# Kernel optimization log

Measured on AMD Instinct MI355X. Metric: run time of the kernel, lower is better.

## Reference

```python
import jax, jax.numpy as jnp
import numpy as np

KEEP_ID, DEL_ID, PAD_ID, STOP_ID, ANNO_ID = 1, 2, 0, 102, 103
V, E, H = 21128, 768, 768
B, T = 8, 256
S = T + 1  # org/simp length; S = T+1 guarantees counters never go out of range


def setup_inputs() -> dict:
    key = jax.random.key(0)
    ks = jax.random.split(key, 16)
    def p(i, shape, scale):
        return jax.random.normal(ks[i], shape, jnp.float32) * scale
    return {
        "input_edits": jax.random.randint(ks[0], (B, T), 0, V),
        "org_ids": jax.random.randint(ks[1], (B, S), 0, V),
        "simp_sent": jax.random.randint(ks[2], (B, S), 0, V),
        "h0": jax.random.normal(ks[3], (B, H), jnp.float32),
        "c0": jax.random.normal(ks[4], (B, H), jnp.float32),
        "encoder_outputs_org": jax.random.normal(ks[5], (B, S, E), jnp.float32),
        "emb": p(6, (V, E), 0.02),
        "Wih_e": p(7, (4 * H, E), 0.03), "Whh_e": p(8, (4 * H, H), 0.03), "b_e": jnp.zeros((4 * H,), jnp.float32),
        "Wih_w": p(9, (4 * H, E), 0.03), "Whh_w": p(10, (4 * H, H), 0.03), "b_w": jnp.zeros((4 * H,), jnp.float32),
        "W_attn": p(11, (H, H), 0.03),
        "W_align": p(12, (H, E), 0.03),
        "W_mlp": p(13, (E, 4 * H), 0.03), "b_mlp": jnp.zeros((E,), jnp.float32),
        "W_out": p(14, (V, E), 0.02), "b_out": jnp.zeros((V,), jnp.float32),
    }


def lstm(x, h0, c0, Wih, Whh, b):
    # x: [B,T,E]; single-layer batch_first LSTM, torch gate order (i,f,g,o)
    def step(carry, xt):
        h, c = carry
        g = xt @ Wih.T + h @ Whh.T + b
        i, f, gg, o = jnp.split(g, 4, axis=-1)
        c2 = jax.nn.sigmoid(f) * c + jax.nn.sigmoid(i) * jnp.tanh(gg)
        h2 = jax.nn.sigmoid(o) * jnp.tanh(c2)
        return (h2, c2), h2
    (hT, cT), hs = jax.lax.scan(step, (h0, c0), jnp.swapaxes(x, 0, 1))
    return jnp.swapaxes(hs, 0, 1), hT, cT


def reference(input_edits, org_ids, simp_sent, h0, c0, encoder_outputs_org,
              emb, Wih_e, Whh_e, b_e, Wih_w, Whh_w, b_w,
              W_attn, W_align, W_mlp, b_mlp, W_out, b_out):
    bsz, nsteps = input_edits.shape
    enc = jnp.tanh(encoder_outputs_org @ W_align.T)            # [B,S,H]
    out_edits, hT, cT = lstm(emb[input_edits], h0, c0, Wih_e, Whh_e, b_e)  # [B,T,H]
    out_words, _, _ = lstm(emb[simp_sent], h0, c0, Wih_w, Whh_w, b_w)      # [B,S,H]

    key = out_edits @ W_attn.T                                  # [B,T,H]
    attn = jax.nn.softmax(jnp.einsum('bth,bsh->bts', key, enc), axis=-1)
    ctx = jnp.einsum('bts,bsh->bth', attn, enc)                 # [B,T,H]

    # counter recurrence (pre-update counters are used for the gathers at step t)
    gold = jnp.swapaxes(input_edits[:, 1:], 0, 1)               # [T-1, B]
    bidx = jnp.arange(bsz)

    def cstep(carry, a):
        kd, ki, an = carry
        kd2 = kd + ((a == KEEP_ID) | (a == DEL_ID)).astype(kd.dtype)
        not_special = (a != DEL_ID) & (a != STOP_ID) & (a != PAD_ID)
        ki2 = ki + not_special.astype(ki.dtype)
        is_ins = not_special & (a != KEEP_ID)
        next_is_anno = org_ids[bidx, an + 1] == ANNO_ID
        an2 = jnp.where(is_ins & next_is_anno, an + 1, jnp.maximum(kd2, an))
        return (kd2, ki2, an2), (ki, an)

    z = jnp.zeros((bsz,), jnp.int32)
    _, (ki_seq, an_seq) = jax.lax.scan(cstep, (z, z, z), gold)
    ki_bt = jnp.swapaxes(ki_seq, 0, 1)                          # [B,T-1]
    an_bt = jnp.swapaxes(an_seq, 0, 1)                          # [B,T-1]

    c = jnp.take_along_axis(enc, an_bt[:, :, None], axis=1)        # [B,T-1,H]
    c_word = jnp.take_along_axis(out_words, ki_bt[:, :, None], axis=1)  # [B,T-1,H]

    Tm1 = nsteps - 1
    feat = jnp.concatenate([out_edits[:, :Tm1], ctx[:, :Tm1], c, c_word], axis=-1)  # [B,T-1,4H]
    mlp = jnp.tanh(feat @ W_mlp.T + b_mlp)                      # [B,T-1,E]
    logp = jax.nn.log_softmax(mlp @ W_out.T + b_out, axis=-1)   # [B,T-1,V]
    return logp, hT, cT
```

## Files before the change

### kernel.cpp

```cpp
#include <hip/hip_runtime.h>
#include <hip/hip_bf16.h>

typedef short s16x8 __attribute__((ext_vector_type(8)));
typedef float f32x4 __attribute__((ext_vector_type(4)));
typedef unsigned short u16;
typedef unsigned short u16x4 __attribute__((ext_vector_type(4)));
typedef unsigned long long u64;
typedef unsigned long long u64x2 __attribute__((ext_vector_type(2)));

__device__ __forceinline__ u16 f2bf(float f) {
  __hip_bfloat16 h = __float2bfloat16(f);
  u16 u;
  __builtin_memcpy(&u, &h, sizeof(u));
  return u;
}
__device__ __forceinline__ float bf2f(u16 u) {
  unsigned int x = ((unsigned int)u) << 16;
  float f;
  __builtin_memcpy(&f, &x, 4);
  return f;
}

__device__ __forceinline__ unsigned int a_ld32(const unsigned int* p) {
  return __hip_atomic_load(p, __ATOMIC_RELAXED, __HIP_MEMORY_SCOPE_AGENT);
}
__device__ __forceinline__ u64 a_ld64(const u64* p) {
  return __hip_atomic_load(p, __ATOMIC_RELAXED, __HIP_MEMORY_SCOPE_AGENT);
}
__device__ __forceinline__ void a_st32(unsigned int* p, unsigned int v) {
  __hip_atomic_store(p, v, __ATOMIC_RELAXED, __HIP_MEMORY_SCOPE_AGENT);
}

__device__ __forceinline__ void gload16(const void* g, void* l) {
  __builtin_amdgcn_global_load_lds(
      (const __attribute__((address_space(1))) unsigned int*)g,
      (__attribute__((address_space(3))) unsigned int*)l, 16, 0, 0);
}

template<int CBF16, int GATHER, int TANHA, int BIAS, int SWAPXY>
__global__ __launch_bounds__(256) void gemm_bt(
    const u16* __restrict__ A, const u16* __restrict__ B,
    const float* __restrict__ bias, void* __restrict__ Cv,
    const int* __restrict__ ids,
    int M, int N, int K, int lda, int ldb, int ldc,
    long sAz, long sBz, long sCz, int rpb, long cbs,
    const int* __restrict__ ids2, const float* __restrict__ bias2, int dM)
{
  __shared__ u16 sA[4096];
  __shared__ u16 sB[4096];
  const int tid = threadIdx.x;
  const int z = blockIdx.z;
  if (z) {
    if (dM) M += dM;
    if (ids2) ids = ids2;
    if (bias2) bias = bias2;
  }
  const int m0 = (SWAPXY ? blockIdx.x : blockIdx.y) * 128;
  const int n0 = (SWAPXY ? blockIdx.y : blockIdx.x) * 128;
  const u16* Ab = A + z * sAz;
  const u16* Bb = B + z * sBz;
  const int w = tid >> 6, lane = tid & 63;
  const int wr = w >> 1, wc = w & 1;
  const int lr = lane & 15, lk = lane >> 4;
  f32x4 acc[4][4] = {};
  const int e0 = tid * 8, e1 = e0 + 2048;
  const int r0 = e0 >> 5, c0 = e0 & 31;
  const int r1 = e1 >> 5, c1 = e1 & 31;
  long arow0, arow1;
  if (GATHER) {
    int i0 = m0 + r0; if (i0 >= M) i0 = M - 1;
    int i1 = m0 + r1; if (i1 >= M) i1 = M - 1;
    arow0 = (long)ids[i0] * lda;
    arow1 = (long)ids[i1] * lda;
  } else {
    arow0 = (long)(m0 + r0) * lda;
    arow1 = (long)(m0 + r1) * lda;
  }
  const long brow0 = (long)(n0 + r0) * ldb;
  const long brow1 = (long)(n0 + r1) * ldb;
  char* sAc = (char*)sA;
  char* sBc = (char*)sB;
  const size_t cb = (size_t)w * 1024;
  for (int kt = 0; kt < K; kt += 32) {
    __syncthreads();
    gload16(Ab + arow0 + kt + c0, sAc + cb);
    gload16(Ab + arow1 + kt + c1, sAc + 4096 + cb);
    gload16(Bb + brow0 + kt + c0, sBc + cb);
    gload16(Bb + brow1 + kt + c1, sBc + 4096 + cb);
    __syncthreads();
    s16x8 af[4], bf[4];
#pragma unroll
    for (int i = 0; i < 4; i++) {
      af[i] = *(const s16x8*)&sA[(wr*64 + i*16 + lr)*32 + lk*8];
      bf[i] = *(const s16x8*)&sB[(wc*64 + i*16 + lr)*32 + lk*8];
    }
#pragma unroll
    for (int mi = 0; mi < 4; mi++)
#pragma unroll
      for (int ni = 0; ni < 4; ni++)
        acc[mi][ni] = __builtin_amdgcn_mfma_f32_16x16x32_bf16(af[mi], bf[ni], acc[mi][ni], 0, 0, 0);
  }
#pragma unroll
  for (int mi = 0; mi < 4; mi++) {
#pragma unroll
    for (int ni = 0; ni < 4; ni++) {
#pragma unroll
      for (int r = 0; r < 4; r++) {
        int gm = m0 + wr*64 + mi*16 + lk*4 + r;
        int gn = n0 + wc*64 + ni*16 + lr;
        if (gm < M && gn < N) {
          float v = acc[mi][ni][r];
          if (BIAS) v += bias[gn];
          if (TANHA) v = tanhf(v);
          long ci = z * sCz + (long)(gm / rpb) * cbs + (long)(gm % rpb) * ldc + gn;
          if (CBF16) ((u16*)Cv)[ci] = f2bf(v);
          else       ((float*)Cv)[ci] = v;
        }
      }
    }
  }
}

__global__ __launch_bounds__(256) void cast_pre(
    const float* __restrict__ emb,
    const float* __restrict__ Wihe, u16* __restrict__ Wihe_bf,
    const float* __restrict__ Wihw, u16* __restrict__ Wihw_bf,
    const float* __restrict__ Walign, u16* __restrict__ Walign_bf,
    const float* __restrict__ encoder, u16* __restrict__ encd_bf,
    u16* __restrict__ gath_bf,
    const int* __restrict__ input_edits, const int* __restrict__ simp_sent,
    const int* __restrict__ org_ids,
    int* __restrict__ ki_bt, int* __restrict__ an_bt,
    unsigned int* __restrict__ tags)
{
  int r = blockIdx.x;
  if (r == 13312) {
    int b = threadIdx.x;
    tags[b] = 0;
    if (b >= 8) return;
    int kd = 0, ki = 0, an = 0;
    for (int t = 0; t < 255; t++) {
      int a = input_edits[b * 256 + t + 1];
      ki_bt[b * 255 + t] = ki;
      an_bt[b * 255 + t] = an;
      int kd2 = kd + ((a == 1) || (a == 2) ? 1 : 0);
      int ns = (a != 2) && (a != 102) && (a != 0);
      int ki2 = ki + (ns ? 1 : 0);
      int is_ins = ns && (a != 1);
      int nia = (org_ids[b * 257 + an + 1] == 103);
      int mx = (kd2 > an) ? kd2 : an;
      int an2 = (is_ins && nia) ? (an + 1) : mx;
      kd = kd2; ki = ki2; an = an2;
    }
    return;
  }
  const float* src; u16* dst; int valid, cols;
  if (r < 3072)                   { src=Wihe + (long)r*768;   dst=Wihe_bf + (long)r*768;   valid=1; cols=768; }
  else if ((r -= 3072) < 3072)    { src=Wihw + (long)r*768;   dst=Wihw_bf + (long)r*768;   valid=1; cols=768; }
  else if ((r -= 3072) < 768)     { src=Walign + (long)r*768; dst=Walign_bf + (long)r*768; valid=1; cols=768; }
  else if ((r -= 768) < 2176)     { src=encoder + (long)r*768; dst=encd_bf + (long)r*768;  valid=(r<2056); cols=768; }
  else if ((r -= 2176) < 2048)    { src=emb + (long)input_edits[r]*768; dst=gath_bf + (long)r*768; valid=1; cols=768; }
  else { r -= 2048;                 int ok=(r<2056);
                                    src=emb + (ok ? (long)simp_sent[r]*768 : 0); 
                                    dst=gath_bf + (long)(2048+r)*768; valid=ok; cols=768; }
  for (int c = threadIdx.x; c < cols; c += 256) {
    float v = valid ? src[c] : 0.f;
    dst[c] = f2bf(v);
  }
}

__global__ __launch_bounds__(256, 1) void lstm_persist(
    const float* __restrict__ Whh_e, const float* __restrict__ Whh_w,
    const float* __restrict__ xW_e, const float* __restrict__ xW_w,
    const float* __restrict__ h0, const float* __restrict__ c0,
    u16* __restrict__ hglob, unsigned int* __restrict__ tags,
    u16* __restrict__ out_e, u16* __restrict__ out_w,
    float* __restrict__ out_tail,
    const float* __restrict__ Wout, u16* __restrict__ Wout_bf,
    const float* __restrict__ Wmlp, u16* __restrict__ Wmlp_bf,
    const float* __restrict__ Wattn, u16* __restrict__ Wattn_bf,
    const u16* __restrict__ enc_bf, u16* __restrict__ encT_bf)
{
  const int wg = blockIdx.x;
  const int tid = threadIdx.x;

  __shared__ u16 ldsh[12288];
  __shared__ float Gbuf[16][4][2][16];

  if (wg >= 48) {
    const int swg = wg - 48;
    u16 (*tile)[33] = (u16(*)[33])ldsh;
    const int TOT = 21248 + 768 + 768 + 1728;
    for (int u = swg; u < TOT; u += 208) {
      if (u < 21248) {
        const float* src = Wout + (long)u * 768;
        u16* dst = Wout_bf + (long)u * 768;
        bool ok = (u < 21128);
        for (int c = tid; c < 768; c += 256)
          dst[c] = f2bf(ok ? src[c] : 0.f);
      } else if (u < 22016) {
        int r = u - 21248;
        const float* src = Wmlp + (long)r * 3072;
        u16* dst = Wmlp_bf + (long)r * 3072;
        for (int c = tid; c < 3072; c += 256)
          dst[c] = f2bf(src[c]);
      } else if (u < 22784) {
        int r = u - 22016;
        const float* src = Wattn + (long)r * 768;
        u16* dst = Wattn_bf + (long)r * 768;
        for (int c = tid; c < 768; c += 256)
          dst[c] = f2bf(src[c]);
      } else {
        int tau = u - 22784;
        int s0 = (tau % 9) * 32;
        int rem = tau / 9;
        int hh0 = (rem % 24) * 32;
        int b = rem / 24;
        const int tx = tid & 31, ty = tid >> 5;
#pragma unroll
        for (int i = 0; i < 32; i += 8) {
          int s = s0 + ty + i;
          u16 v = (s < 257) ? enc_bf[((long)b * 384 + s) * 768 + hh0 + tx] : (u16)0;
          tile[ty + i][tx] = v;
        }
        __syncthreads();
#pragma unroll
        for (int i = 0; i < 32; i += 8) {
          int h = hh0 + ty + i;
          encT_bf[((long)b * 768 + h) * 288 + s0 + tx] = tile[tx][ty + i];
        }
        __syncthreads();
      }
    }
    return;
  }

  const int l = wg / 24, grp = wg % 24;
  const int u0 = grp * 32;
  const int w = tid >> 6, lane = tid & 63;
  const int c16 = lane & 15, half = lane >> 4;
  const int uh = w >> 1, g0 = (w & 1) * 2;

  s16x8 wfrag[2][24];
  {
    const float* Wbase = l ? Whh_w : Whh_e;
#pragma unroll
    for (int g = 0; g < 2; g++) {
      const float* Wsrc = Wbase + (long)((g0 + g) * 768 + u0 + uh * 16 + c16) * 768 + half * 8;
#pragma unroll
      for (int s = 0; s < 24; s++) {
        float4 f0 = *(const float4*)(Wsrc + s * 32);
        float4 f1 = *(const float4*)(Wsrc + s * 32 + 4);
        s16x8 v;
        v[0]=f2bf(f0.x); v[1]=f2bf(f0.y); v[2]=f2bf(f0.z); v[3]=f2bf(f0.w);
        v[4]=f2bf(f1.x); v[5]=f2bf(f1.y); v[6]=f2bf(f1.z); v[7]=f2bf(f1.w);
        wfrag[g][s] = v;
      }
    }
  }

  const int ub = tid >> 4, j2 = (tid & 15) * 2;
  const int uA = u0 + j2;
  float creg0 = 0.f, creg1 = 0.f;
  if (tid < 128) {
    creg0 = c0[ub * 768 + uA];
    creg1 = c0[ub * 768 + uA + 1];
  }

  u16* hg = hglob + l * 24576;
  unsigned int* tg = tags + l * 64;
  const int swA = uA ^ ((ub & 7) << 3);

  if (tid < 128) {
    float v0 = h0[ub * 768 + uA], v1 = h0[ub * 768 + uA + 1];
    u16 h0a = f2bf(v0), h0b = f2bf(v1);
    u16 l0a = f2bf(v0 - bf2f(h0a)), l0b = f2bf(v1 - bf2f(h0b));
    a_st32((unsigned int*)&hg[ub * 768 + swA],
           (unsigned int)h0a | ((unsigned int)h0b << 16));
    a_st32((unsigned int*)&hg[(ub + 8) * 768 + swA],
           (unsigned int)l0a | ((unsigned int)l0b << 16));
  }
  __syncthreads();
  if (tid == 0) a_st32(&tg[grp], 1u);

  const int trow = l ? 257 : 256;
  const float* xrb = (l ? xW_w : xW_e) + ((long)ub * trow) * 3072 + uA;
  u16* outp = (l ? out_w : out_e) + (long)ub * 256 * 768 + uA;
  float2 xq0, xq1, xq2, xq3;
  if (tid < 128) {
    xq0 = *(const float2*)&xrb[0];
    xq1 = *(const float2*)&xrb[768];
    xq2 = *(const float2*)&xrb[1536];
    xq3 = *(const float2*)&xrb[2304];
  }

  for (int t = 0; t < 256; t++) {
    float2 nx0, nx1, nx2, nx3;
    if (tid < 128) {
      const float* xn = xrb + (long)(t + 1) * 3072;
      nx0 = *(const float2*)&xn[0];
      nx1 = *(const float2*)&xn[768];
      nx2 = *(const float2*)&xn[1536];
      nx3 = *(const float2*)&xn[2304];
    }

    {
      const unsigned int tgt = (unsigned int)(t + 1);
      const unsigned int* tp = tg + (t & 1) * 32;
      const bool need = (lane < 24) && (lane != grp);
      while (true) {
        unsigned int v = need ? a_ld32(&tp[lane]) : tgt;
        if (!__any(v < tgt)) break;
        __builtin_amdgcn_s_sleep(1);
      }
      asm volatile("" ::: "memory");
    }

    {
      const u64* hs8 = (const u64*)(hg + (t & 1) * 12288);
#pragma unroll
      for (int i = 0; i < 6; i++) {
        const int idx = i * 256 + tid;
        u64 a = a_ld64(&hs8[idx * 2 + 0]);
        u64 b = a_ld64(&hs8[idx * 2 + 1]);
        u64x2 vv; vv[0] = a; vv[1] = b;
        *(u64x2*)&ldsh[idx * 8] = vv;
      }
    }
    __syncthreads();

    f32x4 acc0 = {}, acc1 = {};
#pragma unroll
    for (int s = 0; s < 24; s++) {
      const int off = (c16 * 768 + s * 32 + half * 8) ^ ((c16 & 7) << 3);
      s16x8 a = *(const s16x8*)&ldsh[off];
      acc0 = __builtin_amdgcn_mfma_f32_16x16x32_bf16(a, wfrag[0][s], acc0, 0, 0, 0);
      acc1 = __builtin_amdgcn_mfma_f32_16x16x32_bf16(a, wfrag[1][s], acc1, 0, 0, 0);
    }
#pragma unroll
    for (int r = 0; r < 4; r++) {
      Gbuf[half * 4 + r][g0 + 0][uh][c16] = acc0[r];
      Gbuf[half * 4 + r][g0 + 1][uh][c16] = acc1[r];
    }
    __syncthreads();

    unsigned int hip = 0;
    float h20 = 0.f, h21 = 0.f, c20 = 0.f, c21 = 0.f;
    if (tid < 128) {
      const int uh0 = j2 >> 4, uc0 = j2 & 15;
      const int uc1 = (j2 + 1) & 15;
      float gi0 = Gbuf[ub][0][uh0][uc0] + Gbuf[ub + 8][0][uh0][uc0] + xq0.x;
      float gf0 = Gbuf[ub][1][uh0][uc0] + Gbuf[ub + 8][1][uh0][uc0] + xq1.x;
      float gg0 = Gbuf[ub][2][uh0][uc0] + Gbuf[ub + 8][2][uh0][uc0] + xq2.x;
      float go0 = Gbuf[ub][3][uh0][uc0] + Gbuf[ub + 8][3][uh0][uc0] + xq3.x;
      float gi1 = Gbuf[ub][0][uh0][uc1] + Gbuf[ub + 8][0][uh0][uc1] + xq0.y;
      float gf1 = Gbuf[ub][1][uh0][uc1] + Gbuf[ub + 8][1][uh0][uc1] + xq1.y;
      float gg1 = Gbuf[ub][2][uh0][uc1] + Gbuf[ub + 8][2][uh0][uc1] + xq2.y;
      float go1 = Gbuf[ub][3][uh0][uc1] + Gbuf[ub + 8][3][uh0][uc1] + xq3.y;
      float si0 = 1.f / (1.f + expf(-gi0)), si1 = 1.f / (1.f + expf(-gi1));
      float sf0 = 1.f / (1.f + expf(-gf0)), sf1 = 1.f / (1.f + expf(-gf1));
      float so0 = 1.f / (1.f + expf(-go0)), so1 = 1.f / (1.f + expf(-go1));
      c20 = sf0 * creg0 + si0 * tanhf(gg0);
      c21 = sf1 * creg1 + si1 * tanhf(gg1);
      h20 = so0 * tanhf(c20);
      h21 = so1 * tanhf(c21);
      creg0 = c20; creg1 = c21;
      u16 hiA = f2bf(h20), hiB = f2bf(h21);
      u16 loA = f2bf(h20 - bf2f(hiA)), loB = f2bf(h21 - bf2f(hiB));
      hip = (unsigned int)hiA | ((unsigned int)hiB << 16);
      unsigned int lop = (unsigned int)loA | ((unsigned int)loB << 16);
      u16* hb = hg + ((t + 1) & 1) * 12288;
      a_st32((unsigned int*)&hb[ub * 768 + swA], hip);
      a_st32((unsigned int*)&hb[(ub + 8) * 768 + swA], lop);
      xq0 = nx0; xq1 = nx1; xq2 = nx2; xq3 = nx3;
    }
    __syncthreads();
    if (tid == 0)
      a_st32(&tg[((t + 1) & 1) * 32 + grp], (unsigned int)(t + 2));

    if (tid < 128) {
      *(unsigned int*)&outp[(long)t * 768] = hip;
      if (l == 0 && t == 255) {
        *(float2*)&out_tail[43101120 + ub * 768 + uA] = make_float2(h20, h21);
        *(float2*)&out_tail[43107264 + ub * 768 + uA] = make_float2(c20, c21);
      }
    }
  }
}

__global__ __launch_bounds__(256) void softmax_k(
    const float* __restrict__ scores, u16* __restrict__ attn)
{
  const int row = blockIdx.x;
  const float* src = scores + (long)row * 288;
  u16* dst = attn + (long)row * 288;
  const int tid = threadIdx.x;
  float v0 = (tid < 257) ? src[tid] : -1e30f;
  float v1 = (tid + 256 < 257) ? src[tid + 256] : -1e30f;
  float mx = fmaxf(v0, v1);
  for (int o = 32; o; o >>= 1) mx = fmaxf(mx, __shfl_xor(mx, o));
  __shared__ float sm[4];
  __shared__ float ss[4];
  if ((tid & 63) == 0) sm[tid >> 6] = mx;
  __syncthreads();
  mx = fmaxf(fmaxf(sm[0], sm[1]), fmaxf(sm[2], sm[3]));
  float e0 = (tid < 257) ? expf(v0 - mx) : 0.f;
  float e1 = (tid + 256 < 257) ? expf(v1 - mx) : 0.f;
  float s = e0 + e1;
  for (int o = 32; o; o >>= 1) s += __shfl_xor(s, o);
  if ((tid & 63) == 0) ss[tid >> 6] = s;
  __syncthreads();
  s = ss[0] + ss[1] + ss[2] + ss[3];
  float inv = 1.f / s;
  dst[tid] = f2bf(e0 * inv);
  if (tid + 256 < 288) dst[tid + 256] = f2bf(e1 * inv);
}

__global__ __launch_bounds__(256) void feat_k(
    const u16* __restrict__ oute, const u16* __restrict__ ctx,
    const u16* __restrict__ encb, const u16* __restrict__ outw,
    const int* __restrict__ ki_bt, const int* __restrict__ an_bt,
    u16* __restrict__ feat)
{
  int q = blockIdx.x * 256 + threadIdx.x;
  int m = q / 768, qq = q - m * 768;
  int seg = qq / 192, off = (qq - seg * 192) * 4;
  u16x4 v = {0, 0, 0, 0};
  if (m < 2040) {
    int b = m / 255, t = m - b * 255;
    const u16* src;
    if (seg == 0)      src = oute + ((long)(b * 256 + t)) * 768 + off;
    else if (seg == 1) src = ctx  + ((long)(b * 256 + t)) * 768 + off;
    else if (seg == 2) src = encb + ((long)(b * 384 + an_bt[m])) * 768 + off;
    else               src = outw + ((long)(b * 256 + ki_bt[m])) * 768 + off;
    v = *(const u16x4*)src;
  }
  *(u16x4*)(feat + (long)q * 4) = v;
}

__global__ __launch_bounds__(256) void logsoftmax_k(float* __restrict__ logits)
{
  const int m = blockIdx.x;
  float* row = logits + (long)m * 21128;
  const int tid = threadIdx.x;
  float mx = -1e30f, sm = 0.f;
  for (int i = tid * 4; i < 21128; i += 1024) {
    float4 v = *(const float4*)(row + i);
    float m4 = fmaxf(fmaxf(v.x, v.y), fmaxf(v.z, v.w));
    if (m4 > mx) { sm *= expf(mx - m4); mx = m4; }
    sm += expf(v.x - mx) + expf(v.y - mx) + expf(v.z - mx) + expf(v.w - mx);
  }
  for (int o = 32; o; o >>= 1) {
    float mo = __shfl_xor(mx, o), so = __shfl_xor(sm, o);
    float nm = fmaxf(mx, mo);
    sm = sm * expf(mx - nm) + so * expf(mo - nm);
    mx = nm;
  }
  __shared__ float wm[4], wsum[4];
  __shared__ float srs;
  if ((tid & 63) == 0) { wm[tid >> 6] = mx; wsum[tid >> 6] = sm; }
  __syncthreads();
  if (tid == 0) {
    float M = wm[0], S = wsum[0];
    for (int i = 1; i < 4; i++) {
      float nm = fmaxf(M, wm[i]);
      S = S * expf(M - nm) + wsum[i] * expf(wm[i] - nm);
      M = nm;
    }
    srs = M + logf(S);
  }
  __syncthreads();
  const float rs = srs;
  for (int i = tid * 4; i < 21128; i += 1024) {
    float4 v = *(const float4*)(row + i);
    v.x -= rs; v.y -= rs; v.z -= rs; v.w -= rs;
    *(float4*)(row + i) = v;
  }
}

extern "C" void kernel_launch(void* const* d_in, const int* in_sizes, int n_in,
                              void* d_out, int out_size, void* d_ws, size_t ws_size,
                              hipStream_t stream) {
  (void)in_sizes; (void)n_in; (void)out_size; (void)ws_size;
  const int*   input_edits = (const int*)d_in[0];
  const int*   org_ids     = (const int*)d_in[1];
  const int*   simp_sent   = (const int*)d_in[2];
  const float* h0      = (const float*)d_in[3];
  const float* c0      = (const float*)d_in[4];
  const float* encoder = (const float*)d_in[5];
  const float* emb     = (const float*)d_in[6];
  const float* Wih_e   = (const float*)d_in[7];
  const float* Whh_e   = (const float*)d_in[8];
  const float* b_e     = (const float*)d_in[9];
  const float* Wih_w   = (const float*)d_in[10];
  const float* Whh_w   = (const float*)d_in[11];
  const float* b_w     = (const float*)d_in[12];
  const float* W_attn  = (const float*)d_in[13];
  const float* W_align = (const float*)d_in[14];
  const float* W_mlp   = (const float*)d_in[15];
  const float* b_mlp   = (const float*)d_in[16];
  const float* W_out   = (const float*)d_in[17];
  const float* b_out   = (const float*)d_in[18];

  float* out = (float*)d_out;
  float* xW_e = out;
  float* xW_w = out + 2048L * 3072;
  u16* encd_bf = (u16*)(out + 2048L * 3072 + 2056L * 3072);
  u16* feat_bf = encd_bf + 2176L * 768;

  char* p = (char*)d_ws;
  auto alloc = [&](size_t bytes) -> char* {
    char* r = p; p += (bytes + 255) & ~(size_t)255; return r;
  };
  u16* Wout_bf   = (u16*)alloc(21248L * 768 * 2);
  u16* Wihe_bf   = (u16*)alloc(3072L * 768 * 2);
  u16* Wihw_bf   = (u16*)alloc(3072L * 768 * 2);
  u16* Wmlp_bf   = (u16*)alloc(768L * 3072 * 2);
  u16* Walign_bf = (u16*)alloc(768L * 768 * 2);
  u16* Wattn_bf  = (u16*)alloc(768L * 768 * 2);
  u16* gath_bf   = (u16*)alloc(4224L * 768 * 2);
  u16* enc_bf    = (u16*)alloc(8L * 384 * 768 * 2);
  u16* encT_bf   = (u16*)alloc(8L * 768 * 288 * 2);
  u16* oute_bf   = (u16*)alloc(2048L * 768 * 2);
  u16* outw_bf   = (u16*)alloc(2048L * 768 * 2);
  u16* key_bf    = (u16*)alloc(2048L * 768 * 2);
  u16* attn_bf   = (u16*)alloc(8L * 256 * 288 * 2);
  u16* ctx_bf    = (u16*)alloc(2048L * 768 * 2);
  u16* mlp_bf    = (u16*)alloc(2048L * 768 * 2);
  float* scores  = (float*)alloc(8L * 256 * 288 * 4);
  u16* hglob     = (u16*)alloc(2L * 2 * 12288 * 2);
  unsigned int* tags = (unsigned int*)alloc(256 * 4);
  int* ki_bt     = (int*)alloc(2040 * 4);
  int* an_bt     = (int*)alloc(2040 * 4);

  dim3 blk(256);
  const int BIGR = 1 << 30;

  cast_pre<<<13313, blk, 0, stream>>>(emb, Wih_e, Wihe_bf, Wih_w, Wihw_bf,
                                      W_align, Walign_bf, encoder, encd_bf,
                                      gath_bf, input_edits, simp_sent,
                                      org_ids, ki_bt, an_bt, tags);

  gemm_bt<1, 0, 1, 0, 0><<<dim3(6, 17, 1), blk, 0, stream>>>(
      encd_bf, Walign_bf, nullptr, enc_bf, nullptr,
      2056, 768, 768, 768, 768, 768, 0, 0, 0, 257, 294912L,
      nullptr, nullptr, 0);

  gemm_bt<0, 0, 0, 1, 0><<<dim3(24, 17, 2), blk, 0, stream>>>(
      gath_bf, Wihe_bf, b_e, xW_e, nullptr,
      2048, 3072, 768, 768, 768, 3072, 1572864L, 2359296L, 6291456L, BIGR, 0,
      nullptr, b_w, 8);

  lstm_persist<<<256, blk, 0, stream>>>(
      Whh_e, Whh_w, xW_e, xW_w, h0, c0, hglob, tags,
      oute_bf, outw_bf, out,
      W_out, Wout_bf, W_mlp, Wmlp_bf, W_attn, Wattn_bf, enc_bf, encT_bf);

  gemm_bt<1, 0, 0, 0, 0><<<dim3(6, 16, 1), blk, 0, stream>>>(
      oute_bf, Wattn_bf, nullptr, key_bf, nullptr,
      2048, 768, 768, 768, 768, 768, 0, 0, 0, BIGR, 0,
      nullptr, nullptr, 0);
  gemm_bt<0, 0, 0, 0, 0><<<dim3(3, 2, 8), blk, 0, stream>>>(
      key_bf, enc_bf, nullptr, scores, nullptr,
      256, 257, 768, 768, 768, 288, 196608L, 294912L, 73728L, BIGR, 0,
      nullptr, nullptr, 0);
  softmax_k<<<2048, blk, 0, stream>>>(scores, attn_bf);
  gemm_bt<1, 0, 0, 0, 0><<<dim3(6, 2, 8), blk, 0, stream>>>(
      attn_bf, encT_bf, nullptr, ctx_bf, nullptr,
      256, 768, 288, 288, 288, 768, 73728L, 221184L, 196608L, BIGR, 0,
      nullptr, nullptr, 0);

  feat_k<<<6144, blk, 0, stream>>>(oute_bf, ctx_bf, enc_bf, outw_bf,
                                   ki_bt, an_bt, feat_bf);
  gemm_bt<1, 0, 1, 1, 0><<<dim3(6, 16, 1), blk, 0, stream>>>(
      feat_bf, Wmlp_bf, b_mlp, mlp_bf, nullptr,
      2040, 768, 3072, 3072, 3072, 768, 0, 0, 0, BIGR, 0,
      nullptr, nullptr, 0);
  gemm_bt<0, 0, 0, 1, 1><<<dim3(16, 166, 1), blk, 0, stream>>>(
      mlp_bf, Wout_bf, b_out, out, nullptr,
      2040, 21128, 768, 768, 768, 21128, 0, 0, 0, BIGR, 0,
      nullptr, nullptr, 0);

  logsoftmax_k<<<2040, blk, 0, stream>>>(out);
}
```

Before: 1.661 ms.

## Fuse attention scores, softmax and context into one kernel; gather MLP features in-GEMM

```diff
diff --git a/kernel.cpp b/kernel.cpp
--- a/kernel.cpp
+++ b/kernel.cpp
@@ -118,6 +118,176 @@
         }
       }
     }
+  }
+}
+
+__global__ __launch_bounds__(256) void gemm_mlp(
+    const u16* __restrict__ oute, const u16* __restrict__ ctxp,
+    const u16* __restrict__ encp, const u16* __restrict__ outw,
+    const int* __restrict__ ki_bt, const int* __restrict__ an_bt,
+    const u16* __restrict__ B, const float* __restrict__ bias,
+    u16* __restrict__ C)
+{
+  __shared__ u16 sA[4096];
+  __shared__ u16 sB[4096];
+  const int tid = threadIdx.x;
+  const int m0 = blockIdx.y * 128, n0 = blockIdx.x * 128;
+  const int w = tid >> 6, lane = tid & 63;
+  const int wr = w >> 1, wc = w & 1;
+  const int lr = lane & 15, lk = lane >> 4;
+  f32x4 acc[4][4] = {};
+  const int e0 = tid * 8, e1 = e0 + 2048;
+  const int r0 = e0 >> 5, c0 = e0 & 31;
+  const int r1 = e1 >> 5, c1 = e1 & 31;
+  const u16 *b00, *b01, *b02, *b03, *b10, *b11, *b12, *b13;
+  {
+    int m = m0 + r0; if (m >= 2040) m = 2039;
+    int b = m / 255, t = m - b * 255;
+    b00 = oute + ((long)(b * 256 + t)) * 768;
+    b01 = ctxp + ((long)(b * 256 + t)) * 768;
+    b02 = encp + ((long)(b * 384 + an_bt[m])) * 768;
+    b03 = outw + ((long)(b * 256 + ki_bt[m])) * 768;
+    m = m0 + r1; if (m >= 2040) m = 2039;
+    b = m / 255; t = m - b * 255;
+    b10 = oute + ((long)(b * 256 + t)) * 768;
+    b11 = ctxp + ((long)(b * 256 + t)) * 768;
+    b12 = encp + ((long)(b * 384 + an_bt[m])) * 768;
+    b13 = outw + ((long)(b * 256 + ki_bt[m])) * 768;
+  }
+  const long brow0 = (long)(n0 + r0) * 3072;
+  const long brow1 = (long)(n0 + r1) * 3072;
+  char* sAc = (char*)sA;
+  char* sBc = (char*)sB;
+  const size_t cb = (size_t)w * 1024;
+  for (int kt = 0; kt < 3072; kt += 32) {
+    const int seg = kt / 768, off = kt - seg * 768;
+    const u16* a0 = (seg == 0 ? b00 : seg == 1 ? b01 : seg == 2 ? b02 : b03) + off + c0;
+    const u16* a1 = (seg == 0 ? b10 : seg == 1 ? b11 : seg == 2 ? b12 : b13) + off + c1;
+    __syncthreads();
+    gload16(a0, sAc + cb);
+    gload16(a1, sAc + 4096 + cb);
+    gload16(B + brow0 + kt + c0, sBc + cb);
+    gload16(B + brow1 + kt + c1, sBc + 4096 + cb);
+    __syncthreads();
+    s16x8 af[4], bf[4];
+#pragma unroll
+    for (int i = 0; i < 4; i++) {
+      af[i] = *(const s16x8*)&sA[(wr*64 + i*16 + lr)*32 + lk*8];
+      bf[i] = *(const s16x8*)&sB[(wc*64 + i*16 + lr)*32 + lk*8];
+    }
+#pragma unroll
+    for (int mi = 0; mi < 4; mi++)
+#pragma unroll
+      for (int ni = 0; ni < 4; ni++)
+        acc[mi][ni] = __builtin_amdgcn_mfma_f32_16x16x32_bf16(af[mi], bf[ni], acc[mi][ni], 0, 0, 0);
+  }
+#pragma unroll
+  for (int mi = 0; mi < 4; mi++) {
+#pragma unroll
+    for (int ni = 0; ni < 4; ni++) {
+#pragma unroll
+      for (int r = 0; r < 4; r++) {
+        int gm = m0 + wr*64 + mi*16 + lk*4 + r;
+        int gn = n0 + wc*64 + ni*16 + lr;
+        if (gm < 2040 && gn < 768) {
+          float v = tanhf(acc[mi][ni][r] + bias[gn]);
+          C[(long)gm * 768 + gn] = f2bf(v);
+        }
+      }
+    }
+  }
+}
+
+__global__ __launch_bounds__(256) void attn_fused(
+    const u16* __restrict__ key, const u16* __restrict__ encb,
+    const u16* __restrict__ encT, u16* __restrict__ ctx)
+{
+  const int b = blockIdx.y;
+  const int w = threadIdx.x >> 6;
+  const int t0 = blockIdx.x * 64 + w * 16;
+  const int lane = threadIdx.x & 63;
+  const int lr = lane & 15, lk = lane >> 4;
+
+  __shared__ u16 plds[4][16][288];
+
+  const u16* arow = key + ((long)(b * 256 + t0 + lr)) * 768 + lk * 8;
+  s16x8 af[24];
+#pragma unroll
+  for (int kt = 0; kt < 24; kt++)
+    af[kt] = *(const s16x8*)(arow + kt * 32);
+
+  f32x4 acc[17];
+  const u16* brow = encb + ((long)(b * 384 + lr)) * 768 + lk * 8;
+#pragma unroll 1
+  for (int nt = 0; nt < 17; nt++) {
+    f32x4 a = {};
+    const u16* bp = brow + (long)nt * 16 * 768;
+#pragma unroll
+    for (int kt = 0; kt < 24; kt++) {
+      s16x8 bf = *(const s16x8*)(bp + kt * 32);
+      a = __builtin_amdgcn_mfma_f32_16x16x32_bf16(af[kt], bf, a, 0, 0, 0);
+    }
+    acc[nt] = a;
+  }
+
+  float sum[4];
+#pragma unroll
+  for (int r = 0; r < 4; r++) {
+    float m = -1e30f;
+#pragma unroll
+    for (int nt = 0; nt < 17; nt++) {
+      bool ok = (nt < 16) || (lr == 0);
+      m = fmaxf(m, ok ? acc[nt][r] : -1e30f);
+    }
+    m = fmaxf(m, __shfl_xor(m, 1));
+    m = fmaxf(m, __shfl_xor(m, 2));
+    m = fmaxf(m, __shfl_xor(m, 4));
+    m = fmaxf(m, __shfl_xor(m, 8));
+    float s = 0.f;
+#pragma unroll
+    for (int nt = 0; nt < 17; nt++) {
+      bool ok = (nt < 16) || (lr == 0);
+      float e = ok ? expf(acc[nt][r] - m) : 0.f;
+      acc[nt][r] = e;
+      s += e;
+    }
+    s += __shfl_xor(s, 1);
+    s += __shfl_xor(s, 2);
+    s += __shfl_xor(s, 4);
+    s += __shfl_xor(s, 8);
+    sum[r] = s;
+  }
+
+#pragma unroll
+  for (int nt = 0; nt < 17; nt++) {
+#pragma unroll
+    for (int r = 0; r < 4; r++)
+      plds[w][lk * 4 + r][nt * 16 + lr] = f2bf(acc[nt][r] / sum[r]);
+  }
+  if (lane < 16) {
+#pragma unroll
+    for (int i = 0; i < 16; i++) plds[w][i][272 + lane] = 0;
+  }
+
+  s16x8 pf[9];
+#pragma unroll
+  for (int ks = 0; ks < 9; ks++)
+    pf[ks] = *(const s16x8*)&plds[w][lr][ks * 32 + lk * 8];
+
+  const u16* browT = encT + ((long)(b * 768 + lr)) * 288 + lk * 8;
+  u16* cbase = ctx + ((long)(b * 256 + t0)) * 768;
+#pragma unroll 1
+  for (int ht = 0; ht < 48; ht++) {
+    f32x4 a = {};
+    const u16* bp = browT + (long)ht * 16 * 288;
+#pragma unroll
+    for (int ks = 0; ks < 9; ks++) {
+      s16x8 bf = *(const s16x8*)(bp + ks * 32);
+      a = __builtin_amdgcn_mfma_f32_16x16x32_bf16(pf[ks], bf, a, 0, 0, 0);
+    }
+#pragma unroll
+    for (int r = 0; r < 4; r++)
+      cbase[(long)(lk * 4 + r) * 768 + ht * 16 + lr] = f2bf(a[r]);
   }
 }
 
@@ -388,56 +558,6 @@
   }
 }
 
-__global__ __launch_bounds__(256) void softmax_k(
-    const float* __restrict__ scores, u16* __restrict__ attn)
-{
-  const int row = blockIdx.x;
-  const float* src = scores + (long)row * 288;
-  u16* dst = attn + (long)row * 288;
-  const int tid = threadIdx.x;
-  float v0 = (tid < 257) ? src[tid] : -1e30f;
-  float v1 = (tid + 256 < 257) ? src[tid + 256] : -1e30f;
-  float mx = fmaxf(v0, v1);
-  for (int o = 32; o; o >>= 1) mx = fmaxf(mx, __shfl_xor(mx, o));
-  __shared__ float sm[4];
-  __shared__ float ss[4];
-  if ((tid & 63) == 0) sm[tid >> 6] = mx;
-  __syncthreads();
-  mx = fmaxf(fmaxf(sm[0], sm[1]), fmaxf(sm[2], sm[3]));
-  float e0 = (tid < 257) ? expf(v0 - mx) : 0.f;
-  float e1 = (tid + 256 < 257) ? expf(v1 - mx) : 0.f;
-  float s = e0 + e1;
-  for (int o = 32; o; o >>= 1) s += __shfl_xor(s, o);
-  if ((tid & 63) == 0) ss[tid >> 6] = s;
-  __syncthreads();
-  s = ss[0] + ss[1] + ss[2] + ss[3];
-  float inv = 1.f / s;
-  dst[tid] = f2bf(e0 * inv);
-  if (tid + 256 < 288) dst[tid + 256] = f2bf(e1 * inv);
-}
-
-__global__ __launch_bounds__(256) void feat_k(
-    const u16* __restrict__ oute, const u16* __restrict__ ctx,
-    const u16* __restrict__ encb, const u16* __restrict__ outw,
-    const int* __restrict__ ki_bt, const int* __restrict__ an_bt,
-    u16* __restrict__ feat)
-{
-  int q = blockIdx.x * 256 + threadIdx.x;
-  int m = q / 768, qq = q - m * 768;
-  int seg = qq / 192, off = (qq - seg * 192) * 4;
-  u16x4 v = {0, 0, 0, 0};
-  if (m < 2040) {
-    int b = m / 255, t = m - b * 255;
-    const u16* src;
-    if (seg == 0)      src = oute + ((long)(b * 256 + t)) * 768 + off;
-    else if (seg == 1) src = ctx  + ((long)(b * 256 + t)) * 768 + off;
-    else if (seg == 2) src = encb + ((long)(b * 384 + an_bt[m])) * 768 + off;
-    else               src = outw + ((long)(b * 256 + ki_bt[m])) * 768 + off;
-    v = *(const u16x4*)src;
-  }
-  *(u16x4*)(feat + (long)q * 4) = v;
-}
-
 __global__ __launch_bounds__(256) void logsoftmax_k(float* __restrict__ logits)
 {
   const int m = blockIdx.x;
@@ -506,7 +626,6 @@
   float* xW_e = out;
   float* xW_w = out + 2048L * 3072;
   u16* encd_bf = (u16*)(out + 2048L * 3072 + 2056L * 3072);
-  u16* feat_bf = encd_bf + 2176L * 768;
 
   char* p = (char*)d_ws;
   auto alloc = [&](size_t bytes) -> char* {
@@ -524,14 +643,12 @@
   u16* oute_bf   = (u16*)alloc(2048L * 768 * 2);
   u16* outw_bf   = (u16*)alloc(2048L * 768 * 2);
   u16* key_bf    = (u16*)alloc(2048L * 768 * 2);
-  u16* attn_bf   = (u16*)alloc(8L * 256 * 288 * 2);
   u16* ctx_bf    = (u16*)alloc(2048L * 768 * 2);
   u16* mlp_bf    = (u16*)alloc(2048L * 768 * 2);
-  float* scores  = (float*)alloc(8L * 256 * 288 * 4);
   u16* hglob     = (u16*)alloc(2L * 2 * 12288 * 2);
   unsigned int* tags = (unsigned int*)alloc(256 * 4);
-  int* ki_bt     = (int*)alloc(2040 * 4);
-  int* an_bt     = (int*)alloc(2040 * 4);
+  int* ki_bt     = (int*)alloc(2048 * 4);
+  int* an_bt     = (int*)alloc(2048 * 4);
 
   dim3 blk(256);
   const int BIGR = 1 << 30;
@@ -560,22 +677,12 @@
       oute_bf, Wattn_bf, nullptr, key_bf, nullptr,
       2048, 768, 768, 768, 768, 768, 0, 0, 0, BIGR, 0,
       nullptr, nullptr, 0);
-  gemm_bt<0, 0, 0, 0, 0><<<dim3(3, 2, 8), blk, 0, stream>>>(
-      key_bf, enc_bf, nullptr, scores, nullptr,
-      256, 257, 768, 768, 768, 288, 196608L, 294912L, 73728L, BIGR, 0,
-      nullptr, nullptr, 0);
-  softmax_k<<<2048, blk, 0, stream>>>(scores, attn_bf);
-  gemm_bt<1, 0, 0, 0, 0><<<dim3(6, 2, 8), blk, 0, stream>>>(
-      attn_bf, encT_bf, nullptr, ctx_bf, nullptr,
-      256, 768, 288, 288, 288, 768, 73728L, 221184L, 196608L, BIGR, 0,
-      nullptr, nullptr, 0);
-
-  feat_k<<<6144, blk, 0, stream>>>(oute_bf, ctx_bf, enc_bf, outw_bf,
-                                   ki_bt, an_bt, feat_bf);
-  gemm_bt<1, 0, 1, 1, 0><<<dim3(6, 16, 1), blk, 0, stream>>>(
-      feat_bf, Wmlp_bf, b_mlp, mlp_bf, nullptr,
-      2040, 768, 3072, 3072, 3072, 768, 0, 0, 0, BIGR, 0,
-      nullptr, nullptr, 0);
+  attn_fused<<<dim3(4, 8), blk, 0, stream>>>(key_bf, enc_bf, encT_bf, ctx_bf);
+
+  gemm_mlp<<<dim3(6, 16), blk, 0, stream>>>(
+      oute_bf, ctx_bf, enc_bf, outw_bf, ki_bt, an_bt,
+      Wmlp_bf, b_mlp, mlp_bf);
+
   gemm_bt<0, 0, 0, 1, 1><<<dim3(16, 166, 1), blk, 0, stream>>>(
       mlp_bf, Wout_bf, b_out, out, nullptr,
       2040, 21128, 768, 768, 768, 21128, 0, 0, 0, BIGR, 0,
```

New measurement: 1.726 ms. 3.9% more time.
